# Performance work log

Measured on AMD Instinct MI355X. Metric: run time of the kernel, lower is better.

## Reference

```python
import jax, jax.numpy as jnp
import numpy as np

B, S, DIM = 2, 2048, 2048
NH, NKV = 32, 8
HD = DIM // NH  # 64


def setup_inputs() -> dict:
    key = jax.random.key(0)
    ks = jax.random.split(key, 6)
    x = jax.random.normal(ks[0], (B, S, DIM), jnp.float32)
    # realistic rotary tables: [S, HD//2]
    inv_freq = 1.0 / (10000.0 ** (jnp.arange(0, HD, 2, dtype=jnp.float32) / HD))
    freqs = jnp.arange(S, dtype=jnp.float32)[:, None] * inv_freq[None, :]
    cos, sin = jnp.cos(freqs), jnp.sin(freqs)
    init = lambda k, shape: jax.random.normal(k, shape, jnp.float32) * (shape[0] ** -0.5)
    Wq = init(ks[1], (DIM, NH * HD))
    Wk = init(ks[2], (DIM, NKV * HD))
    Wv = init(ks[3], (DIM, NKV * HD))
    Wo = init(ks[4], (NH * HD, DIM))
    return {"x": x, "cos": cos, "sin": sin, "Wq": Wq, "Wk": Wk, "Wv": Wv, "Wo": Wo}


def _rope(t, c, s):
    # t: [B, S, H, HD]; c, s: [1, S, 1, HD//2]; consecutive-pair (v1) style
    b, sl, h, hd = t.shape
    tp = t.reshape(b, sl, h, hd // 2, 2)
    t0, t1 = tp[..., 0], tp[..., 1]
    return jnp.stack([t0 * c - t1 * s, t0 * s + t1 * c], axis=-1).reshape(b, sl, h, hd)


def reference(x, cos, sin, Wq, Wk, Wv, Wo):
    b, sl, _ = x.shape
    q = (x @ Wq).reshape(b, sl, NH, HD)
    k = (x @ Wk).reshape(b, sl, NKV, HD)
    v = (x @ Wv).reshape(b, sl, NKV, HD)
    c = cos[None, :, None, :]
    s = sin[None, :, None, :]
    q = _rope(q, c, s)
    k = _rope(k, c, s)
    n_rep = NH // NKV
    k = jnp.repeat(k, n_rep, axis=2)  # GQA repeat_interleave over heads
    v = jnp.repeat(v, n_rep, axis=2)
    scale = 1.0 / np.sqrt(HD)
    scores = jnp.einsum("bqhd,bkhd->bhqk", q, k) * scale  # [B, H, S, S]
    causal = jnp.tril(jnp.ones((sl, sl), dtype=bool))
    scores = jnp.where(causal[None, None], scores, -jnp.inf)
    p = jax.nn.softmax(scores, axis=-1)
    out = jnp.einsum("bhqk,bkhd->bqhd", p, v).reshape(b, sl, NH * HD)
    return out @ Wo
```

## Files before the change

### kernel.cpp

```cpp
#include <hip/hip_runtime.h>
#include <hip/hip_bf16.h>


typedef __attribute__((ext_vector_type(8))) short short8;
typedef __attribute__((ext_vector_type(4))) float f32x4;
typedef __attribute__((ext_vector_type(16))) float f32x16;
typedef __attribute__((ext_vector_type(2))) int i32x2;
typedef __attribute__((ext_vector_type(4))) int i32x4;

__device__ __forceinline__ unsigned short f2bfu(float f){
  unsigned u = __float_as_uint(f);
  u += 0x7FFFu + ((u >> 16) & 1u);
  return (unsigned short)(u >> 16);
}
__device__ __forceinline__ float bfu2f(unsigned short u){
  return __uint_as_float(((unsigned)u) << 16);
}
__device__ __forceinline__ unsigned cvt_pk_bf16(float lo, float hi){
  unsigned r;
  asm("v_cvt_pk_bf16_f32 %0, %1, %2" : "=v"(r) : "v"(lo), "v"(hi));
  return r;
}
__device__ __forceinline__ i32x2 pl32swap(int a, int b){
  auto r = __builtin_amdgcn_permlane32_swap(a, b, false, false);
  return __builtin_bit_cast(i32x2, r);
}
__device__ __forceinline__ int swz64(int row, int slot){
  return row * 64 + (((slot) ^ (row & 7)) << 3);
}
template<int N> __device__ __forceinline__ void vm_wait(){
  if constexpr (N == 10)      asm volatile("s_waitcnt vmcnt(10)" ::: "memory");
  else if constexpr (N == 8)  asm volatile("s_waitcnt vmcnt(8)" ::: "memory");
  else if constexpr (N == 7)  asm volatile("s_waitcnt vmcnt(7)" ::: "memory");
  else if constexpr (N == 6)  asm volatile("s_waitcnt vmcnt(6)" ::: "memory");
  else if constexpr (N == 5)  asm volatile("s_waitcnt vmcnt(5)" ::: "memory");
  else if constexpr (N == 4)  asm volatile("s_waitcnt vmcnt(4)" ::: "memory");
  else if constexpr (N == 3)  asm volatile("s_waitcnt vmcnt(3)" ::: "memory");
  else if constexpr (N == 2)  asm volatile("s_waitcnt vmcnt(2)" ::: "memory");
  else                        asm volatile("s_waitcnt vmcnt(0)" ::: "memory");
}

__global__ void convx_kernel(const float* __restrict__ x, unsigned short* __restrict__ xb, int n4){
  int i = blockIdx.x * blockDim.x + threadIdx.x;
  if (i >= n4) return;
  float4 v = reinterpret_cast<const float4*>(x)[i];
  ushort4 o;
  o.x = f2bfu(v.x); o.y = f2bfu(v.y); o.z = f2bfu(v.z); o.w = f2bfu(v.w);
  reinterpret_cast<ushort4*>(xb)[i] = o;
}

__global__ void transpose_conv_kernel(const float* __restrict__ in, unsigned short* __restrict__ out,
                                      int Min, int Nin){
  __shared__ float t[32][33];
  int c0 = blockIdx.x * 32, r0 = blockIdx.y * 32;
  int tx = threadIdx.x, ty = threadIdx.y;
  #pragma unroll
  for (int i = ty; i < 32; i += 8) t[i][tx] = in[(size_t)(r0 + i) * Nin + c0 + tx];
  __syncthreads();
  #pragma unroll
  for (int i = ty; i < 32; i += 8) out[(size_t)(c0 + i) * Min + r0 + tx] = f2bfu(t[tx][i]);
}

#define PH4(SLOT,KK,VMW,...) { \
  const unsigned short* sAc = &sA[SLOT][(KK)*4096]; \
  const unsigned short* sBc = &sB[SLOT][(KK)*RB]; \
  short8 afr[4]; short8 bfr[6]; \
  _Pragma("unroll") for (int m_ = 0; m_ < 4; m_++) \
    afr[m_] = *reinterpret_cast<const short8*>(sAc + aOff[m_]); \
  _Pragma("unroll") for (int n_ = 0; n_ < NFR; n_++) \
    bfr[n_] = *reinterpret_cast<const short8*>(sBc + bOff[n_]); \
  __VA_ARGS__; \
  __builtin_amdgcn_s_barrier(); \
  asm volatile("s_waitcnt lgkmcnt(0)" ::: "memory"); \
  __builtin_amdgcn_sched_barrier(0); \
  __builtin_amdgcn_s_setprio(1); \
  _Pragma("unroll") for (int m_ = 0; m_ < 4; m_++){ \
    _Pragma("unroll") for (int n_ = 0; n_ < NFR; n_++){ \
      acc[m_][n_] = __builtin_amdgcn_mfma_f32_16x16x32_bf16(afr[m_], bfr[n_], acc[m_][n_], 0, 0, 0); }} \
  __builtin_amdgcn_s_setprio(0); \
  VMW; \
  __builtin_amdgcn_s_barrier(); \
}

template<int NF, bool OUTBF16>
__global__ __launch_bounds__(256, 2) void gemm4p_kernel(const unsigned short* __restrict__ A,
                                                        const unsigned short* __restrict__ B,
                                                        void* __restrict__ Cp,
                                                        int M, int N, int K, int nbx){
  constexpr int NFR = 2 * NF;
  constexpr int RB  = NF * 2048;
  constexpr int VMS = 2 * (2 + NF);
  __shared__ unsigned short sA[2][8192];
  __shared__ unsigned short sB[2][2 * RB];
  const int tid = threadIdx.x;
  const int l = tid & 63, w = tid >> 6;
  const int quad = l >> 4, c16 = l & 15;
  const int cpx = (int)gridDim.x >> 3;
  const int id2 = ((int)blockIdx.x & 7) * cpx + ((int)blockIdx.x >> 3);
  const int bx = id2 % nbx, by = id2 / nbx;
  const int row0 = by * 128, col0 = bx * (NF * 64);
  const int wr = w >> 1, wc = w & 1;

  const unsigned short* gAp[2];
  const unsigned short* gBp[NF];
  #pragma unroll
  for (int j = 0; j < 2; j++){
    int rl = w * 32 + j * 16 + (l >> 2);
    gAp[j] = A + (size_t)(row0 + rl) * K + ((((l & 3) ^ ((rl >> 1) & 3))) << 3);
  }
  #pragma unroll
  for (int j = 0; j < NF; j++){
    int rl = w * (16 * NF) + j * 16 + (l >> 2);
    gBp[j] = B + (size_t)(col0 + rl) * K + ((((l & 3) ^ ((rl >> 1) & 3))) << 3);
  }

  auto stA = [&](int slot, int kk, int col){
    #pragma unroll
    for (int j = 0; j < 2; j++)
      __builtin_amdgcn_global_load_lds((const __attribute__((address_space(1))) void*)(gAp[j] + col),
          (__attribute__((address_space(3))) void*)(&sA[slot][kk * 4096 + w * 1024 + j * 512]), 16, 0, 0);
  };
  auto stB = [&](int slot, int kk, int col){
    #pragma unroll
    for (int j = 0; j < NF; j++)
      __builtin_amdgcn_global_load_lds((const __attribute__((address_space(1))) void*)(gBp[j] + col),
          (__attribute__((address_space(3))) void*)(&sB[slot][kk * RB + w * (512 * NF) + j * 512]), 16, 0, 0);
  };

  int aOff[4], bOff[6];
  #pragma unroll
  for (int mf = 0; mf < 4; mf++){
    int row = wr * 64 + mf * 16 + c16;
    aOff[mf] = row * 32 + ((quad ^ ((row >> 1) & 3)) << 3);
  }
  #pragma unroll
  for (int nf = 0; nf < NFR; nf++){
    int row = wc * (NF * 32) + nf * 16 + c16;
    bOff[nf] = row * 32 + ((quad ^ ((row >> 1) & 3)) << 3);
  }

  stA(0, 0, 0);  stB(0, 0, 0);
  stA(0, 1, 32); stB(0, 1, 32);
  stA(1, 0, 64); stB(1, 0, 64);
  vm_wait<VMS>();
  __builtin_amdgcn_s_barrier();

  f32x4 acc[4][6] = {};
  const int NI = K >> 7;
  #pragma unroll 1
  for (int j = 0; j < NI - 1; ++j){
    const int t1c  = (2 * j + 1) * 64 + 32;
    const int t2c0 = (2 * j + 2) * 64;
    const int t2c1 = t2c0 + 32;
    const int t3c0 = (2 * j + 3) * 64;
    PH4(0,0, vm_wait<VMS>(), stA(1,1,t1c);  stB(1,1,t1c))
    PH4(0,1, vm_wait<VMS>(), stA(0,0,t2c0); stB(0,0,t2c0))
    PH4(1,0, vm_wait<VMS>(), stA(0,1,t2c1); stB(0,1,t2c1))
    PH4(1,1, vm_wait<VMS>(), stA(1,0,t3c0); stB(1,0,t3c0))
  }
  {
    const int t1c = K - 32;
    PH4(0,0, vm_wait<VMS>(), stA(1,1,t1c); stB(1,1,t1c))
    PH4(0,1, vm_wait<0>(), ;)
    PH4(1,0, vm_wait<0>(), ;)
    PH4(1,1, (void)0, ;)
  }

  #pragma unroll
  for (int mf = 0; mf < 4; mf++)
    #pragma unroll
    for (int nf = 0; nf < NFR; nf++)
      #pragma unroll
      for (int r = 0; r < 4; r++){
        size_t off = (size_t)(row0 + wr * 64 + mf * 16 + quad * 4 + r) * N + (col0 + wc * (NF * 32) + nf * 16 + c16);
        if (OUTBF16) ((unsigned short*)Cp)[off] = f2bfu(acc[mf][nf][r]);
        else         ((float*)Cp)[off] = acc[mf][nf][r];
      }
}

__global__ void rope_kernel(const unsigned short* __restrict__ qkv, const float* __restrict__ cosb,
                            const float* __restrict__ sinb, unsigned short* __restrict__ Qo,
                            unsigned short* __restrict__ Ko){
  int idx = blockIdx.x * 256 + threadIdx.x;
  const int NQ = 4096 * 1024;
  if (idx < NQ){
    int m = idx >> 10, p = idx & 1023;
    int h = p >> 5, i = p & 31;
    int s = m & 2047;
    unsigned pr = *reinterpret_cast<const unsigned*>(qkv + (size_t)m * 3072 + h * 64 + 2 * i);
    float t0 = bfu2f((unsigned short)(pr & 0xFFFFu));
    float t1 = bfu2f((unsigned short)(pr >> 16));
    float c = cosb[s * 32 + i], sn = sinb[s * 32 + i];
    const float SC = 0.18033688011112042f;
    float o0 = (t0 * c - t1 * sn) * SC;
    float o1 = (t0 * sn + t1 * c) * SC;
    unsigned ow = (unsigned)f2bfu(o0) | ((unsigned)f2bfu(o1) << 16);
    *reinterpret_cast<unsigned*>(Qo + (size_t)m * 2048 + h * 64 + 2 * i) = ow;
  } else {
    int j = idx - NQ;
    int m = j >> 8, p = j & 255;
    int kvh = p >> 5, i = p & 31;
    int s = m & 2047, b = m >> 11;
    unsigned pr = *reinterpret_cast<const unsigned*>(qkv + (size_t)m * 3072 + 2048 + kvh * 64 + 2 * i);
    float t0 = bfu2f((unsigned short)(pr & 0xFFFFu));
    float t1 = bfu2f((unsigned short)(pr >> 16));
    float c = cosb[s * 32 + i], sn = sinb[s * 32 + i];
    float o0 = t0 * c - t1 * sn;
    float o1 = t0 * sn + t1 * c;
    unsigned ow = (unsigned)f2bfu(o0) | ((unsigned)f2bfu(o1) << 16);
    *reinterpret_cast<unsigned*>(Ko + ((size_t)(b * 8 + kvh) * 2048 + s) * 64 + 2 * i) = ow;
  }
}

__global__ void vtrans_kernel(const unsigned short* __restrict__ qkv, unsigned short* __restrict__ Vt){
  __shared__ float t[64][65];
  int bh = blockIdx.y;
  int s0 = blockIdx.x * 64;
  int b = bh >> 3, kvh = bh & 7;
  int tid = threadIdx.x;
  #pragma unroll
  for (int it = 0; it < 16; it++){
    int id = it * 256 + tid;
    int sl = id >> 6, d = id & 63;
    unsigned short u = qkv[(size_t)(b * 2048 + s0 + sl) * 3072 + 2560 + kvh * 64 + d];
    t[sl][d] = bfu2f(u);
  }
  __syncthreads();
  #pragma unroll
  for (int it = 0; it < 16; it++){
    int id = it * 256 + tid;
    int dl = id >> 6, sl = id & 63;
    Vt[((size_t)(b * 8 + kvh) * 64 + dl) * 2048 + s0 + sl] = f2bfu(t[sl][dl]);
  }
}

__global__ __launch_bounds__(256, 4) void attn_kernel(const unsigned short* __restrict__ Q,
                                                      const unsigned short* __restrict__ Kt,
                                                      const unsigned short* __restrict__ Vt,
                                                      unsigned short* __restrict__ O){
  __shared__ unsigned short sK[2][64 * 64];
  __shared__ unsigned short sV[2][64 * 64];
  const int tid = threadIdx.x;
  const int l = tid & 63, w = tid >> 6;
  const int q32 = l & 31, hi = l >> 5;
  const int bid = blockIdx.x;
  const int qt = 15 - (bid >> 6);
  const int bh = bid & 63;
  const int b = bh >> 5, h = bh & 31, kvh = h >> 2;
  const int q0w = qt * 128 + w * 32;
  const int nt = 2 * qt + 2;

  const unsigned short* Kb = Kt + (size_t)(b * 8 + kvh) * 2048 * 64;
  const unsigned short* Vb = Vt + (size_t)(b * 8 + kvh) * 64 * 2048;

  auto stage = [&](int kv0, int buf){
    #pragma unroll
    for (int c = 0; c < 2; c++){
      const int rl = w * 16 + c * 8 + (l >> 3);
      const int ce = (((l & 7) ^ (l >> 3)) << 3);
      __builtin_amdgcn_global_load_lds(
        (const __attribute__((address_space(1))) void*)(Kb + (size_t)(kv0 + rl) * 64 + ce),
        (__attribute__((address_space(3))) void*)(&sK[buf][(w * 16 + c * 8) * 64]), 16, 0, 0);
      __builtin_amdgcn_global_load_lds(
        (const __attribute__((address_space(1))) void*)(Vb + (size_t)rl * 2048 + kv0 + ce),
        (__attribute__((address_space(3))) void*)(&sV[buf][(w * 16 + c * 8) * 64]), 16, 0, 0);
    }
  };

  short8 qv[4];
  {
    const unsigned short* Qp = Q + (size_t)(b * 2048 + q0w + q32) * 2048 + h * 64 + hi * 8;
    #pragma unroll
    for (int kd = 0; kd < 4; kd++) qv[kd] = *reinterpret_cast<const short8*>(Qp + kd * 16);
  }

  const short8 ones = {0x3F80, 0x3F80, 0x3F80, 0x3F80, 0x3F80, 0x3F80, 0x3F80, 0x3F80};

  f32x16 accA = {}, accB = {};
  f32x16 accl = {};

#define MKAP(Z, R0, AP) { \
    unsigned A_ = cvt_pk_bf16(Z[R0+0], Z[R0+1]); \
    unsigned B_ = cvt_pk_bf16(Z[R0+2], Z[R0+3]); \
    unsigned C_ = cvt_pk_bf16(Z[R0+4], Z[R0+5]); \
    unsigned D_ = cvt_pk_bf16(Z[R0+6], Z[R0+7]); \
    i32x2 s1_ = pl32swap((int)A_, (int)C_); \
    i32x2 s2_ = pl32swap((int)B_, (int)D_); \
    i32x4 q_ = {s1_[0], s2_[0], s1_[1], s2_[1]}; \
    AP = __builtin_bit_cast(short8, q_); \
  }

  stage(0, 0);
  vm_wait<0>();
  __builtin_amdgcn_s_barrier();

  for (int t = 0; t < nt; ++t){
    const int kv0 = t * 64;
    const int buf = t & 1;
    if (t + 1 < nt) stage((t + 1) * 64, buf ^ 1);

    const unsigned short* sKc = &sK[buf][0];
    const unsigned short* sVc = &sV[buf][0];

    f32x16 z0 = {}, z1 = {};
    __builtin_amdgcn_s_setprio(1);
    #pragma unroll
    for (int kd = 0; kd < 4; kd++){
      const int u = kd * 2 + hi;
      short8 ak0 = *reinterpret_cast<const short8*>(&sKc[swz64(q32, u)]);
      short8 ak1 = *reinterpret_cast<const short8*>(&sKc[swz64(32 + q32, u)]);
      z0 = __builtin_amdgcn_mfma_f32_32x32x16_bf16(ak0, qv[kd], z0, 0, 0, 0);
      z1 = __builtin_amdgcn_mfma_f32_32x32x16_bf16(ak1, qv[kd], z1, 0, 0, 0);
    }
    __builtin_amdgcn_s_setprio(0);

    if (kv0 + 63 > q0w){
      const int qg = q0w + q32;
      #pragma unroll
      for (int r = 0; r < 16; r++){
        const int kr = (r & 3) + 8 * (r >> 2) + 4 * hi;
        if (kv0 + kr > qg)      z0[r] = -1e30f;
        if (kv0 + 32 + kr > qg) z1[r] = -1e30f;
      }
    }

    #pragma unroll
    for (int r = 0; r < 16; r++){
      z0[r] = __builtin_amdgcn_exp2f(z0[r]);
      z1[r] = __builtin_amdgcn_exp2f(z1[r]);
    }

    short8 apA, apB;
    __builtin_amdgcn_s_setprio(1);
    MKAP(z0, 0, apA)
    MKAP(z0, 8, apB)
    accl = __builtin_amdgcn_mfma_f32_32x32x16_bf16(apA, ones, accl, 0, 0, 0);
    accl = __builtin_amdgcn_mfma_f32_32x32x16_bf16(apB, ones, accl, 0, 0, 0);
    {
      short8 bv;
      bv = *reinterpret_cast<const short8*>(&sVc[swz64(q32, 0 * 2 + hi)]);
      accA = __builtin_amdgcn_mfma_f32_32x32x16_bf16(apA, bv, accA, 0, 0, 0);
      bv = *reinterpret_cast<const short8*>(&sVc[swz64(q32, 1 * 2 + hi)]);
      accA = __builtin_amdgcn_mfma_f32_32x32x16_bf16(apB, bv, accA, 0, 0, 0);
      bv = *reinterpret_cast<const short8*>(&sVc[swz64(32 + q32, 0 * 2 + hi)]);
      accB = __builtin_amdgcn_mfma_f32_32x32x16_bf16(apA, bv, accB, 0, 0, 0);
      bv = *reinterpret_cast<const short8*>(&sVc[swz64(32 + q32, 1 * 2 + hi)]);
      accB = __builtin_amdgcn_mfma_f32_32x32x16_bf16(apB, bv, accB, 0, 0, 0);
    }
    MKAP(z1, 0, apA)
    MKAP(z1, 8, apB)
    accl = __builtin_amdgcn_mfma_f32_32x32x16_bf16(apA, ones, accl, 0, 0, 0);
    accl = __builtin_amdgcn_mfma_f32_32x32x16_bf16(apB, ones, accl, 0, 0, 0);
    {
      short8 bv;
      bv = *reinterpret_cast<const short8*>(&sVc[swz64(q32, 2 * 2 + hi)]);
      accA = __builtin_amdgcn_mfma_f32_32x32x16_bf16(apA, bv, accA, 0, 0, 0);
      bv = *reinterpret_cast<const short8*>(&sVc[swz64(q32, 3 * 2 + hi)]);
      accA = __builtin_amdgcn_mfma_f32_32x32x16_bf16(apB, bv, accA, 0, 0, 0);
      bv = *reinterpret_cast<const short8*>(&sVc[swz64(32 + q32, 2 * 2 + hi)]);
      accB = __builtin_amdgcn_mfma_f32_32x32x16_bf16(apA, bv, accB, 0, 0, 0);
      bv = *reinterpret_cast<const short8*>(&sVc[swz64(32 + q32, 3 * 2 + hi)]);
      accB = __builtin_amdgcn_mfma_f32_32x32x16_bf16(apB, bv, accB, 0, 0, 0);
    }
    __builtin_amdgcn_s_setprio(0);

    vm_wait<0>();
    __builtin_amdgcn_s_barrier();
  }
#undef MKAP

  #pragma unroll
  for (int r = 0; r < 16; r++){
    const float inv = 1.0f / accl[r];
    const int qrow = q0w + (r & 3) + 8 * (r >> 2) + 4 * hi;
    const size_t base = (size_t)(b * 2048 + qrow) * 2048 + h * 64 + q32;
    O[base]      = f2bfu(accA[r] * inv);
    O[base + 32] = f2bfu(accB[r] * inv);
  }
}

extern "C" void kernel_launch(void* const* d_in, const int* in_sizes, int n_in,
                              void* d_out, int out_size, void* d_ws, size_t ws_size,
                              hipStream_t stream){
  (void)in_sizes; (void)n_in; (void)out_size; (void)ws_size;
  const float* x  = (const float*)d_in[0];
  const float* cb = (const float*)d_in[1];
  const float* sb = (const float*)d_in[2];
  const float* Wq = (const float*)d_in[3];
  const float* Wk = (const float*)d_in[4];
  const float* Wv = (const float*)d_in[5];
  const float* Wo = (const float*)d_in[6];
  float* out = (float*)d_out;
  char* ws = (char*)d_ws;

  unsigned short* qkv = (unsigned short*)(ws + 0);
  unsigned short* xb  = (unsigned short*)(ws + 25165824);
  unsigned short* wt  = (unsigned short*)(ws + 41943040);
  unsigned short* qb  = (unsigned short*)(ws + 54525952);
  unsigned short* kb  = (unsigned short*)(ws + 71303168);
  unsigned short* vt  = (unsigned short*)(ws + 75497472);

  dim3 tb(32, 8);
  convx_kernel<<<8192, 256, 0, stream>>>(x, xb, 2097152);
  transpose_conv_kernel<<<dim3(64, 64), tb, 0, stream>>>(Wq, wt, 2048, 2048);
  transpose_conv_kernel<<<dim3(16, 64), tb, 0, stream>>>(Wk, wt + (size_t)2048 * 2048, 2048, 512);
  transpose_conv_kernel<<<dim3(16, 64), tb, 0, stream>>>(Wv, wt + (size_t)2560 * 2048, 2048, 512);
  gemm4p_kernel<3, true><<<512, 256, 0, stream>>>(xb, wt, qkv, 4096, 3072, 2048, 16);
  rope_kernel<<<20480, 256, 0, stream>>>(qkv, cb, sb, qb, kb);
  vtrans_kernel<<<dim3(32, 16), 256, 0, stream>>>(qkv, vt);
  transpose_conv_kernel<<<dim3(64, 64), tb, 0, stream>>>(Wo, wt, 2048, 2048);
  attn_kernel<<<1024, 256, 0, stream>>>(qb, kb, vt, xb);
  gemm4p_kernel<2, false><<<512, 256, 0, stream>>>(xb, wt, out, 4096, 2048, 2048, 16);
}
```

Measured before the change: 188.4 us.

## Fuse Q RoPE into attention, merge weight transposes and K/V prep kernels

Q rotary embedding and scaling now happen inside the attention kernel when Q fragments are loaded straight from the qkv buffer. This removes the separate Q write and read, about 16 MB of bf16 traffic. All four weight transpose-converts become one launch, with Wo written to its own buffer so it no longer has to wait until after the QKV GEMM. K RoPE and the V transpose are merged into a single kernel. Together these cut launch count and memory traffic, at the cost of a little extra ALU work and cos/sin loads in the attention prologue.

```diff
diff --git a/kernel.cpp b/kernel.cpp
--- a/kernel.cpp
+++ b/kernel.cpp
@@ -49,16 +49,23 @@
   reinterpret_cast<ushort4*>(xb)[i] = o;
 }
 
-__global__ void transpose_conv_kernel(const float* __restrict__ in, unsigned short* __restrict__ out,
-                                      int Min, int Nin){
+__global__ void wtrans_all_kernel(const float* __restrict__ Wq, const float* __restrict__ Wk,
+                                  const float* __restrict__ Wv, const float* __restrict__ Wo,
+                                  unsigned short* __restrict__ wt, unsigned short* __restrict__ wot){
   __shared__ float t[32][33];
-  int c0 = blockIdx.x * 32, r0 = blockIdx.y * 32;
+  int tile = blockIdx.x;
+  const float* in; unsigned short* out; int Nin, bx;
+  if (tile < 4096)      { in = Wq; out = wt;                          Nin = 2048; bx = tile & 63;  tile >>= 6; }
+  else if (tile < 5120) { in = Wk; out = wt + (size_t)2048 * 2048;    Nin = 512;  tile -= 4096; bx = tile & 15; tile >>= 4; }
+  else if (tile < 6144) { in = Wv; out = wt + (size_t)2560 * 2048;    Nin = 512;  tile -= 5120; bx = tile & 15; tile >>= 4; }
+  else                  { in = Wo; out = wot;                         Nin = 2048; tile -= 6144; bx = tile & 63; tile >>= 6; }
+  const int c0 = bx * 32, r0 = tile * 32;
   int tx = threadIdx.x, ty = threadIdx.y;
   #pragma unroll
   for (int i = ty; i < 32; i += 8) t[i][tx] = in[(size_t)(r0 + i) * Nin + c0 + tx];
   __syncthreads();
   #pragma unroll
-  for (int i = ty; i < 32; i += 8) out[(size_t)(c0 + i) * Min + r0 + tx] = f2bfu(t[tx][i]);
+  for (int i = ty; i < 32; i += 8) out[(size_t)(c0 + i) * 2048 + r0 + tx] = f2bfu(t[tx][i]);
 }
 
 #define PH4(SLOT,KK,VMW,...) { \
@@ -178,26 +185,14 @@
       }
 }
 
-__global__ void rope_kernel(const unsigned short* __restrict__ qkv, const float* __restrict__ cosb,
-                            const float* __restrict__ sinb, unsigned short* __restrict__ Qo,
-                            unsigned short* __restrict__ Ko){
-  int idx = blockIdx.x * 256 + threadIdx.x;
-  const int NQ = 4096 * 1024;
-  if (idx < NQ){
-    int m = idx >> 10, p = idx & 1023;
-    int h = p >> 5, i = p & 31;
-    int s = m & 2047;
-    unsigned pr = *reinterpret_cast<const unsigned*>(qkv + (size_t)m * 3072 + h * 64 + 2 * i);
-    float t0 = bfu2f((unsigned short)(pr & 0xFFFFu));
-    float t1 = bfu2f((unsigned short)(pr >> 16));
-    float c = cosb[s * 32 + i], sn = sinb[s * 32 + i];
-    const float SC = 0.18033688011112042f;
-    float o0 = (t0 * c - t1 * sn) * SC;
-    float o1 = (t0 * sn + t1 * c) * SC;
-    unsigned ow = (unsigned)f2bfu(o0) | ((unsigned)f2bfu(o1) << 16);
-    *reinterpret_cast<unsigned*>(Qo + (size_t)m * 2048 + h * 64 + 2 * i) = ow;
-  } else {
-    int j = idx - NQ;
+__global__ void prep_kv_kernel(const unsigned short* __restrict__ qkv, const float* __restrict__ cosb,
+                               const float* __restrict__ sinb, unsigned short* __restrict__ Ko,
+                               unsigned short* __restrict__ Vt){
+  __shared__ float t[64][65];
+  const int blk = blockIdx.x;
+  const int tid = threadIdx.x;
+  if (blk < 4096){
+    int j = blk * 256 + tid;
     int m = j >> 8, p = j & 255;
     int kvh = p >> 5, i = p & 31;
     int s = m & 2047, b = m >> 11;
@@ -209,32 +204,29 @@
     float o1 = t0 * sn + t1 * c;
     unsigned ow = (unsigned)f2bfu(o0) | ((unsigned)f2bfu(o1) << 16);
     *reinterpret_cast<unsigned*>(Ko + ((size_t)(b * 8 + kvh) * 2048 + s) * 64 + 2 * i) = ow;
-  }
-}
-
-__global__ void vtrans_kernel(const unsigned short* __restrict__ qkv, unsigned short* __restrict__ Vt){
-  __shared__ float t[64][65];
-  int bh = blockIdx.y;
-  int s0 = blockIdx.x * 64;
-  int b = bh >> 3, kvh = bh & 7;
-  int tid = threadIdx.x;
-  #pragma unroll
-  for (int it = 0; it < 16; it++){
-    int id = it * 256 + tid;
-    int sl = id >> 6, d = id & 63;
-    unsigned short u = qkv[(size_t)(b * 2048 + s0 + sl) * 3072 + 2560 + kvh * 64 + d];
-    t[sl][d] = bfu2f(u);
-  }
-  __syncthreads();
-  #pragma unroll
-  for (int it = 0; it < 16; it++){
-    int id = it * 256 + tid;
-    int dl = id >> 6, sl = id & 63;
-    Vt[((size_t)(b * 8 + kvh) * 64 + dl) * 2048 + s0 + sl] = f2bfu(t[sl][dl]);
-  }
-}
-
-__global__ __launch_bounds__(256, 4) void attn_kernel(const unsigned short* __restrict__ Q,
+  } else {
+    const int bid2 = blk - 4096;
+    const int s0 = (bid2 & 31) * 64, bh = bid2 >> 5;
+    const int b = bh >> 3, kvh = bh & 7;
+    #pragma unroll
+    for (int it = 0; it < 16; it++){
+      int id = it * 256 + tid;
+      int sl = id >> 6, d = id & 63;
+      t[sl][d] = bfu2f(qkv[(size_t)(b * 2048 + s0 + sl) * 3072 + 2560 + kvh * 64 + d]);
+    }
+    __syncthreads();
+    #pragma unroll
+    for (int it = 0; it < 16; it++){
+      int id = it * 256 + tid;
+      int dl = id >> 6, sl = id & 63;
+      Vt[((size_t)(b * 8 + kvh) * 64 + dl) * 2048 + s0 + sl] = f2bfu(t[sl][dl]);
+    }
+  }
+}
+
+__global__ __launch_bounds__(256, 4) void attn_kernel(const unsigned short* __restrict__ qkv,
+                                                      const float* __restrict__ cosb,
+                                                      const float* __restrict__ sinb,
                                                       const unsigned short* __restrict__ Kt,
                                                       const unsigned short* __restrict__ Vt,
                                                       unsigned short* __restrict__ O){
@@ -269,9 +261,27 @@
 
   short8 qv[4];
   {
-    const unsigned short* Qp = Q + (size_t)(b * 2048 + q0w + q32) * 2048 + h * 64 + hi * 8;
-    #pragma unroll
-    for (int kd = 0; kd < 4; kd++) qv[kd] = *reinterpret_cast<const short8*>(Qp + kd * 16);
+    const int s = q0w + q32;
+    const unsigned short* Qp = qkv + (size_t)(b * 2048 + s) * 3072 + h * 64 + hi * 8;
+    const float* cp = cosb + s * 32 + hi * 4;
+    const float* sp = sinb + s * 32 + hi * 4;
+    const float SC = 0.18033688011112042f;
+    #pragma unroll
+    for (int kd = 0; kd < 4; kd++){
+      short8 raw = *reinterpret_cast<const short8*>(Qp + kd * 16);
+      float4 c4 = *reinterpret_cast<const float4*>(cp + kd * 8);
+      float4 s4 = *reinterpret_cast<const float4*>(sp + kd * 8);
+      unsigned pk[4];
+      #pragma unroll
+      for (int j = 0; j < 4; j++){
+        float t0 = bfu2f((unsigned short)raw[2 * j]);
+        float t1 = bfu2f((unsigned short)raw[2 * j + 1]);
+        float cc = (&c4.x)[j], sn = (&s4.x)[j];
+        pk[j] = cvt_pk_bf16((t0 * cc - t1 * sn) * SC, (t0 * sn + t1 * cc) * SC);
+      }
+      i32x4 q_ = {(int)pk[0], (int)pk[1], (int)pk[2], (int)pk[3]};
+      qv[kd] = __builtin_bit_cast(short8, q_);
+    }
   }
 
   const short8 ones = {0x3F80, 0x3F80, 0x3F80, 0x3F80, 0x3F80, 0x3F80, 0x3F80, 0x3F80};
@@ -396,19 +406,15 @@
   unsigned short* qkv = (unsigned short*)(ws + 0);
   unsigned short* xb  = (unsigned short*)(ws + 25165824);
   unsigned short* wt  = (unsigned short*)(ws + 41943040);
-  unsigned short* qb  = (unsigned short*)(ws + 54525952);
+  unsigned short* wot = (unsigned short*)(ws + 54525952);
   unsigned short* kb  = (unsigned short*)(ws + 71303168);
   unsigned short* vt  = (unsigned short*)(ws + 75497472);
 
   dim3 tb(32, 8);
   convx_kernel<<<8192, 256, 0, stream>>>(x, xb, 2097152);
-  transpose_conv_kernel<<<dim3(64, 64), tb, 0, stream>>>(Wq, wt, 2048, 2048);
-  transpose_conv_kernel<<<dim3(16, 64), tb, 0, stream>>>(Wk, wt + (size_t)2048 * 2048, 2048, 512);
-  transpose_conv_kernel<<<dim3(16, 64), tb, 0, stream>>>(Wv, wt + (size_t)2560 * 2048, 2048, 512);
+  wtrans_all_kernel<<<10240, tb, 0, stream>>>(Wq, Wk, Wv, Wo, wt, wot);
   gemm4p_kernel<3, true><<<512, 256, 0, stream>>>(xb, wt, qkv, 4096, 3072, 2048, 16);
-  rope_kernel<<<20480, 256, 0, stream>>>(qkv, cb, sb, qb, kb);
-  vtrans_kernel<<<dim3(32, 16), 256, 0, stream>>>(qkv, vt);
-  transpose_conv_kernel<<<dim3(64, 64), tb, 0, stream>>>(Wo, wt, 2048, 2048);
-  attn_kernel<<<1024, 256, 0, stream>>>(qb, kb, vt, xb);
-  gemm4p_kernel<2, false><<<512, 256, 0, stream>>>(xb, wt, out, 4096, 2048, 2048, 16);
-}
+  prep_kv_kernel<<<4608, 256, 0, stream>>>(qkv, cb, sb, kb, vt);
+  attn_kernel<<<1024, 256, 0, stream>>>(qkv, cb, sb, kb, vt, xb);
+  gemm4p_kernel<2, false><<<512, 256, 0, stream>>>(xb, wot, out, 4096, 2048, 2048, 16);
+}
```

Measured after the change: 176.9 us. -6.1%, faster.
